# Kernel optimization log

Hardware: AMD Instinct MI355X
Metric: run time of the kernel (lower is better)

Reference implementation:

```python
import jax, jax.numpy as jnp
import numpy as np

B, S, DIM, HID = 2, 256, 128, 128
EPS = 1e-5

def _ln(t, w, b):
    mu = jnp.mean(t, axis=-1, keepdims=True)
    var = jnp.mean(jnp.square(t - mu), axis=-1, keepdims=True)
    return (t - mu) * jax.lax.rsqrt(var + EPS) * w + b

def setup_inputs() -> dict:
    key = jax.random.key(0)
    ks = jax.random.split(key, 8)
    sc = 1.0 / np.sqrt(DIM)
    return {
        "x": jax.random.normal(ks[0], (B, S, S, DIM), dtype=jnp.float32),
        "mask": jax.random.uniform(ks[1], (B, S, S), dtype=jnp.float32),
        "norm_w": jnp.ones((DIM,), jnp.float32),
        "norm_b": jnp.zeros((DIM,), jnp.float32),
        "w_left": jax.random.uniform(ks[2], (HID, DIM), jnp.float32, -sc, sc),
        "w_right": jax.random.uniform(ks[3], (HID, DIM), jnp.float32, -sc, sc),
        "w_lg": jax.random.uniform(ks[4], (HID, DIM), jnp.float32, -sc, sc),
        "w_rg": jax.random.uniform(ks[5], (HID, DIM), jnp.float32, -sc, sc),
        "w_og": jax.random.uniform(ks[6], (HID, DIM), jnp.float32, -sc, sc),
        "out_norm_w": jnp.ones((HID,), jnp.float32),
        "out_norm_b": jnp.zeros((HID,), jnp.float32),
        "w_out": jax.random.uniform(ks[7], (DIM, HID), jnp.float32, -1.0 / np.sqrt(HID), 1.0 / np.sqrt(HID)),
    }

def reference(x, mask, norm_w, norm_b, w_left, w_right, w_lg, w_rg, w_og,
              out_norm_w, out_norm_b, w_out):
    xn = _ln(x, norm_w, norm_b)                      # [B,S,S,D]
    m = mask[..., None]                              # [B,S,S,1]
    left = (xn @ w_left.T) * m * jax.nn.sigmoid(xn @ w_lg.T)    # [B,S,S,H]
    right = (xn @ w_right.T) * m * jax.nn.sigmoid(xn @ w_rg.T)  # [B,S,S,H]
    out_gate = jax.nn.sigmoid(xn @ w_og.T)
    # torch: permute to [B,H,S,S], bf16 bmm, permute back -> out[b,i,j,h] = sum_k L[b,i,k,h]*R[b,j,k,h]
    out = jnp.einsum("bikh,bjkh->bijh",
                     left.astype(jnp.bfloat16), right.astype(jnp.bfloat16),
                     preferred_element_type=jnp.float32)
    out = out.astype(jnp.bfloat16).astype(jnp.float32)
    out = _ln(out, out_norm_w, out_norm_b) * out_gate
    return out @ w_out.T                             # [B,S,S,D]
```

## Files before the change

kernel.cpp:

```cpp
#include <hip/hip_runtime.h>


#define SS 256
#define DD 128
#define HH 128

typedef __attribute__((ext_vector_type(8))) short bf16x8;
typedef __attribute__((ext_vector_type(4))) float f32x4;

__device__ __forceinline__ unsigned short f2b(float f) {
  unsigned u = __builtin_bit_cast(unsigned, f);
  u = (u + 0x7FFFu + ((u >> 16) & 1u)) >> 16;
  return (unsigned short)u;
}
__device__ __forceinline__ float b2f(unsigned short h) {
  return __builtin_bit_cast(float, ((unsigned)h) << 16);
}
__device__ __forceinline__ float sigmoidf_(float x) {
  return 1.0f / (1.0f + expf(-x));
}

__global__ __launch_bounds__(1024) void k_cvt(
    const float* __restrict__ s0, const float* __restrict__ s1,
    const float* __restrict__ s2, const float* __restrict__ s3,
    const float* __restrict__ s4, const float* __restrict__ s5,
    unsigned short* __restrict__ dst)
{
  int m = blockIdx.x >> 4;
  int e = ((blockIdx.x & 15) << 10) | threadIdx.x;
  const float* s = (m == 0) ? s0 : (m == 1) ? s1 : (m == 2) ? s2
                 : (m == 3) ? s3 : (m == 4) ? s4 : s5;
  dst[m * 16384 + e] = f2b(s[e]);
}

__global__ __launch_bounds__(256, 4) void k_stage1(
    const float* __restrict__ x, const float* __restrict__ mask,
    const float* __restrict__ nw, const float* __restrict__ nb,
    const unsigned short* __restrict__ wb,
    unsigned short* __restrict__ Lt, unsigned short* __restrict__ Rt,
    unsigned short* __restrict__ og)
{
  __shared__ unsigned short xnS[64][136];
  __shared__ unsigned short oS[128][72];
  __shared__ float maskS[64];

  const int tid  = threadIdx.x;
  const int wave = tid >> 6, lane = tid & 63;
  const int quad = lane >> 4, l16 = lane & 15;
  const int r0 = blockIdx.x * 64;
  const int bq = r0 >> 16, iq = (r0 >> 8) & 255, j0 = r0 & 255;

  if (tid < 64) maskS[tid] = mask[r0 + tid];

  const float w0 = nw[lane], w1 = nw[lane + 64];
  const float b0 = nb[lane], b1 = nb[lane + 64];
  float v0a[16], v1a[16];
  #pragma unroll
  for (int rr = 0; rr < 16; ++rr) {
    const float* xr = x + (size_t)(r0 + wave * 16 + rr) * DD;
    v0a[rr] = xr[lane];
    v1a[rr] = xr[lane + 64];
  }
  #pragma unroll
  for (int rr = 0; rr < 16; ++rr) {
    int r = wave * 16 + rr;
    float v0 = v0a[rr], v1 = v1a[rr];
    float s = v0 + v1;
    #pragma unroll
    for (int o = 32; o; o >>= 1) s += __shfl_xor(s, o);
    float mu = s * (1.0f / 128.0f);
    float d0 = v0 - mu, d1 = v1 - mu;
    float q = d0 * d0 + d1 * d1;
    #pragma unroll
    for (int o = 32; o; o >>= 1) q += __shfl_xor(q, o);
    float rs = rsqrtf(q * (1.0f / 128.0f) + 1e-5f);
    xnS[r][lane]      = f2b(d0 * rs * w0 + b0);
    xnS[r][lane + 64] = f2b(d1 * rs * w1 + b1);
  }
  __syncthreads();

  const int h0 = wave * 32;
  const int jl = quad * 4;

  auto coopStore = [&](unsigned short* dstBase) {
    int h = tid >> 1, half = tid & 1;
    const bf16x8* s = (const bf16x8*)&oS[h][half * 32];
    bf16x8* d = (bf16x8*)(dstBase +
        ((((size_t)bq * 128 + h) * 256 + iq) * 256 + j0 + half * 32));
    d[0] = s[0]; d[1] = s[1]; d[2] = s[2]; d[3] = s[3];
  };

  auto gatedSection = [&](const unsigned short* __restrict__ Wv,
                          const unsigned short* __restrict__ Wg) {
    const unsigned short* pv = Wv + (h0 + l16) * 128 + quad * 8;
    const unsigned short* pg = Wg + (h0 + l16) * 128 + quad * 8;
    f32x4 aV[4][2], aG[4][2];
    #pragma unroll
    for (int rt = 0; rt < 4; ++rt)
      #pragma unroll
      for (int n = 0; n < 2; ++n) {
        aV[rt][n] = f32x4{0.f, 0.f, 0.f, 0.f};
        aG[rt][n] = f32x4{0.f, 0.f, 0.f, 0.f};
      }
    bf16x8 bv[2], bg[2], bvn[2], bgn[2];
    #pragma unroll
    for (int n = 0; n < 2; ++n) {
      bv[n] = *(const bf16x8*)(pv + n * 2048);
      bg[n] = *(const bf16x8*)(pg + n * 2048);
    }
    #pragma unroll
    for (int kk = 0; kk < 4; ++kk) {
      if (kk < 3) {
        #pragma unroll
        for (int n = 0; n < 2; ++n) {
          bvn[n] = *(const bf16x8*)(pv + n * 2048 + (kk + 1) * 32);
          bgn[n] = *(const bf16x8*)(pg + n * 2048 + (kk + 1) * 32);
        }
      }
      #pragma unroll
      for (int rt = 0; rt < 4; ++rt) {
        bf16x8 a = *(const bf16x8*)&xnS[rt * 16 + l16][kk * 32 + quad * 8];
        #pragma unroll
        for (int n = 0; n < 2; ++n) {
          aG[rt][n] = __builtin_amdgcn_mfma_f32_16x16x32_bf16(a, bg[n], aG[rt][n], 0, 0, 0);
          aV[rt][n] = __builtin_amdgcn_mfma_f32_16x16x32_bf16(a, bv[n], aV[rt][n], 0, 0, 0);
        }
      }
      #pragma unroll
      for (int n = 0; n < 2; ++n) { bv[n] = bvn[n]; bg[n] = bgn[n]; }
    }
    #pragma unroll
    for (int rt = 0; rt < 4; ++rt)
      #pragma unroll
      for (int n = 0; n < 2; ++n)
        #pragma unroll
        for (int rg = 0; rg < 4; ++rg) {
          float g = sigmoidf_(aG[rt][n][rg]);
          oS[h0 + n * 16 + l16][rt * 16 + jl + rg] =
              f2b(aV[rt][n][rg] * maskS[rt * 16 + jl + rg] * g);
        }
  };

  gatedSection(wb + 0 * 16384, wb + 2 * 16384);
  __syncthreads();
  coopStore(Lt);
  __syncthreads();

  gatedSection(wb + 1 * 16384, wb + 3 * 16384);
  __syncthreads();
  coopStore(Rt);
  __syncthreads();

  {
    const unsigned short* po = wb + 4 * 16384 + (h0 + l16) * 128 + quad * 8;
    f32x4 aO[4][2];
    #pragma unroll
    for (int rt = 0; rt < 4; ++rt)
      #pragma unroll
      for (int n = 0; n < 2; ++n) aO[rt][n] = f32x4{0.f, 0.f, 0.f, 0.f};
    bf16x8 bo[2], bon[2];
    #pragma unroll
    for (int n = 0; n < 2; ++n) bo[n] = *(const bf16x8*)(po + n * 2048);
    #pragma unroll
    for (int kk = 0; kk < 4; ++kk) {
      if (kk < 3) {
        #pragma unroll
        for (int n = 0; n < 2; ++n)
          bon[n] = *(const bf16x8*)(po + n * 2048 + (kk + 1) * 32);
      }
      #pragma unroll
      for (int rt = 0; rt < 4; ++rt) {
        bf16x8 a = *(const bf16x8*)&xnS[rt * 16 + l16][kk * 32 + quad * 8];
        #pragma unroll
        for (int n = 0; n < 2; ++n)
          aO[rt][n] = __builtin_amdgcn_mfma_f32_16x16x32_bf16(a, bo[n], aO[rt][n], 0, 0, 0);
      }
      #pragma unroll
      for (int n = 0; n < 2; ++n) bo[n] = bon[n];
    }
    unsigned short* ogS = &oS[0][0];
    #pragma unroll
    for (int rt = 0; rt < 4; ++rt)
      #pragma unroll
      for (int n = 0; n < 2; ++n)
        #pragma unroll
        for (int rg = 0; rg < 4; ++rg)
          ogS[(rt * 16 + jl + rg) * 136 + h0 + n * 16 + l16] =
              f2b(sigmoidf_(aO[rt][n][rg]));
  }
  __syncthreads();
  {
    int j = tid >> 2, qq = tid & 3;
    const bf16x8* s = (const bf16x8*)&oS[0][0] + 0;
    const unsigned short* ogS = &oS[0][0];
    const bf16x8* sp = (const bf16x8*)&ogS[j * 136 + qq * 32];
    bf16x8* d = (bf16x8*)(og + (size_t)(r0 + j) * HH + qq * 32);
    d[0] = sp[0]; d[1] = sp[1]; d[2] = sp[2]; d[3] = sp[3];
    (void)s;
  }
}

__global__ __launch_bounds__(256, 4) void k_stage2(
    const unsigned short* __restrict__ Lt, const unsigned short* __restrict__ Rt,
    unsigned short* __restrict__ Tt)
{
  __shared__ unsigned short As[128][72];
  __shared__ unsigned short Bs[128][72];

  const int tid  = threadIdx.x;
  const int wave = tid >> 6, lane = tid & 63;
  const int quad = lane >> 4, l16 = lane & 15;
  const int bh = blockIdx.y;
  const int it = blockIdx.x >> 1, jt = blockIdx.x & 1;

  const unsigned short* A  = Lt + (size_t)bh * 65536 + it * 128 * 256;
  const unsigned short* Bp = Rt + (size_t)bh * 65536 + jt * 128 * 256;

  f32x4 acc[2][8];
  #pragma unroll
  for (int mt = 0; mt < 2; ++mt)
    #pragma unroll
    for (int nt = 0; nt < 8; ++nt) acc[mt][nt] = f32x4{0.f, 0.f, 0.f, 0.f};

  const int srow = tid >> 3, sc8 = tid & 7;

  #pragma unroll
  for (int ks = 0; ks < 4; ++ks) {
    __syncthreads();
    #pragma unroll
    for (int i = 0; i < 4; ++i) {
      *(bf16x8*)&As[i * 32 + srow][sc8 * 8] =
          *(const bf16x8*)(A + (i * 32 + srow) * 256 + ks * 64 + sc8 * 8);
      *(bf16x8*)&Bs[i * 32 + srow][sc8 * 8] =
          *(const bf16x8*)(Bp + (i * 32 + srow) * 256 + ks * 64 + sc8 * 8);
    }
    __syncthreads();
    #pragma unroll
    for (int k2 = 0; k2 < 2; ++k2) {
      int ko = k2 * 32 + quad * 8;
      bf16x8 a0 = *(const bf16x8*)&As[wave * 32 + l16][ko];
      bf16x8 a1 = *(const bf16x8*)&As[wave * 32 + 16 + l16][ko];
      #pragma unroll
      for (int nt = 0; nt < 8; ++nt) {
        bf16x8 b = *(const bf16x8*)&Bs[nt * 16 + l16][ko];
        acc[0][nt] = __builtin_amdgcn_mfma_f32_16x16x32_bf16(a0, b, acc[0][nt], 0, 0, 0);
        acc[1][nt] = __builtin_amdgcn_mfma_f32_16x16x32_bf16(a1, b, acc[1][nt], 0, 0, 0);
      }
    }
  }

  unsigned short* C = Tt + (size_t)bh * 65536 + it * 128 * 256 + jt * 128;
  #pragma unroll
  for (int mt = 0; mt < 2; ++mt)
    #pragma unroll
    for (int nt = 0; nt < 8; ++nt)
      #pragma unroll
      for (int rg = 0; rg < 4; ++rg)
        C[(wave * 32 + mt * 16 + quad * 4 + rg) * 256 + nt * 16 + l16] = f2b(acc[mt][nt][rg]);
}

__global__ __launch_bounds__(256, 4) void k_stage3(
    const unsigned short* __restrict__ Tt, const unsigned short* __restrict__ og,
    const float* __restrict__ onw, const float* __restrict__ onb,
    const unsigned short* __restrict__ wbO, float* __restrict__ out)
{
  __shared__ unsigned short tS[128][72];
  __shared__ unsigned short vS[64][136];
  __shared__ float onwS[128], onbS[128];
  __shared__ float muS[64], rsS[64];

  const int tid  = threadIdx.x;
  const int wave = tid >> 6, lane = tid & 63;
  const int quad = lane >> 4, l16 = lane & 15;
  const int r0 = blockIdx.x * 64;
  const int bq = r0 >> 16, iq = (r0 >> 8) & 255, j0 = r0 & 255;

  if (tid < 128) { onwS[tid] = onw[tid]; onbS[tid] = onb[tid]; }

  {
    int h = tid >> 1, half = tid & 1;
    const bf16x8* s = (const bf16x8*)(Tt +
        ((((size_t)bq * 128 + h) * 256 + iq) * 256 + j0 + half * 32));
    bf16x8* d = (bf16x8*)&tS[h][half * 32];
    d[0] = s[0]; d[1] = s[1]; d[2] = s[2]; d[3] = s[3];
  }
  __syncthreads();

  {
    int j = lane;
    #pragma unroll
    for (int c = 0; c < 4; ++c) {
      bf16x8 t;
      #pragma unroll
      for (int e = 0; e < 8; ++e) t[e] = (short)tS[wave * 32 + c * 8 + e][j];
      *(bf16x8*)&vS[j][wave * 32 + c * 8] = t;
    }
  }
  __syncthreads();

  if (tid < 128) {
    int j = tid >> 1, h0 = (tid & 1) * 64;
    float s = 0.f, q = 0.f;
    #pragma unroll
    for (int h = 0; h < 64; ++h) {
      float v = b2f(vS[j][h0 + h]);
      s += v; q += v * v;
    }
    s += __shfl_xor(s, 1);
    q += __shfl_xor(q, 1);
    float mu = s * (1.0f / 128.0f);
    float var = q * (1.0f / 128.0f) - mu * mu;
    float rs = rsqrtf(var + 1e-5f);
    if ((tid & 1) == 0) { muS[j] = mu; rsS[j] = rs; }
  }
  __syncthreads();

  {
    int j = tid >> 2, hq = tid & 3;
    float mu = muS[j], rs = rsS[j];
    const unsigned short* ogp = og + (size_t)(r0 + j) * HH + hq * 32;
    unsigned short* vp = &vS[j][hq * 32];
    #pragma unroll
    for (int c = 0; c < 4; ++c) {
      bf16x8 tv = *(bf16x8*)&vp[c * 8];
      bf16x8 gv = *(const bf16x8*)(ogp + c * 8);
      bf16x8 r;
      #pragma unroll
      for (int e = 0; e < 8; ++e) {
        int hh = hq * 32 + c * 8 + e;
        float v = (b2f((unsigned short)tv[e]) - mu) * rs * onwS[hh] + onbS[hh];
        r[e] = (short)f2b(v * b2f((unsigned short)gv[e]));
      }
      *(bf16x8*)&vp[c * 8] = r;
    }
  }
  __syncthreads();

  f32x4 acc[8];
  #pragma unroll
  for (int nt = 0; nt < 8; ++nt) acc[nt] = f32x4{0.f, 0.f, 0.f, 0.f};
  #pragma unroll
  for (int kk = 0; kk < 4; ++kk) {
    bf16x8 a = *(const bf16x8*)&vS[wave * 16 + l16][kk * 32 + quad * 8];
    #pragma unroll
    for (int nt = 0; nt < 8; ++nt) {
      bf16x8 b = *(const bf16x8*)(wbO + (nt * 16 + l16) * 128 + kk * 32 + quad * 8);
      acc[nt] = __builtin_amdgcn_mfma_f32_16x16x32_bf16(a, b, acc[nt], 0, 0, 0);
    }
  }
  #pragma unroll
  for (int nt = 0; nt < 8; ++nt)
    #pragma unroll
    for (int rg = 0; rg < 4; ++rg)
      out[(size_t)(r0 + wave * 16 + quad * 4 + rg) * DD + nt * 16 + l16] = acc[nt][rg];
}

extern "C" void kernel_launch(void* const* d_in, const int* in_sizes, int n_in,
                              void* d_out, int out_size, void* d_ws, size_t ws_size,
                              hipStream_t stream)
{
  const float* x    = (const float*)d_in[0];
  const float* mask = (const float*)d_in[1];
  const float* nw   = (const float*)d_in[2];
  const float* nb   = (const float*)d_in[3];
  const float* wL   = (const float*)d_in[4];
  const float* wR   = (const float*)d_in[5];
  const float* wLG  = (const float*)d_in[6];
  const float* wRG  = (const float*)d_in[7];
  const float* wOG  = (const float*)d_in[8];
  const float* onw  = (const float*)d_in[9];
  const float* onb  = (const float*)d_in[10];
  const float* wO   = (const float*)d_in[11];

  char* ws = (char*)d_ws;
  unsigned short* wb = (unsigned short*)ws;
  unsigned short* og = (unsigned short*)(ws + (1 << 18));
  unsigned short* Lt = (unsigned short*)(ws + (1 << 18) + 1 * (size_t)(1 << 25));
  unsigned short* Rt = (unsigned short*)(ws + (1 << 18) + 2 * (size_t)(1 << 25));
  unsigned short* Tt = (unsigned short*)(ws + (1 << 18) + 3 * (size_t)(1 << 25));

  k_cvt<<<96, 1024, 0, stream>>>(wL, wR, wLG, wRG, wOG, wO, wb);
  k_stage1<<<2048, 256, 0, stream>>>(x, mask, nw, nb, wb, Lt, Rt, og);
  k_stage2<<<dim3(4, 256), 256, 0, stream>>>(Lt, Rt, Tt);
  k_stage3<<<2048, 256, 0, stream>>>(Tt, og, onw, onb, wb + 5 * 16384, (float*)d_out);
}
```

Baseline: 275.2 us.

## Prefetch stage2 tiles into registers, remap blocks per XCD, make stage3 wave-local

Stage2 now loads the next K-slice from global memory into registers while MFMAs run on the current shared-memory tile. It also remaps block indices so blocks sharing the same L/R panels land on the same XCD, aiming for better L2 reuse. Stage3 is restructured so each wave owns its 16 rows end to end: layer-norm stats are computed per wave and passed by shuffle, the gate load is prefetched early, and block-wide barriers become waitcnt fences. This cuts synchronisation and latency, at the cost of higher register pressure and a reliance on wave-local data ownership for correctness.

```diff
diff --git a/kernel.cpp b/kernel.cpp
--- a/kernel.cpp
+++ b/kernel.cpp
@@ -191,12 +191,10 @@
   __syncthreads();
   {
     int j = tid >> 2, qq = tid & 3;
-    const bf16x8* s = (const bf16x8*)&oS[0][0] + 0;
     const unsigned short* ogS = &oS[0][0];
     const bf16x8* sp = (const bf16x8*)&ogS[j * 136 + qq * 32];
     bf16x8* d = (bf16x8*)(og + (size_t)(r0 + j) * HH + qq * 32);
     d[0] = sp[0]; d[1] = sp[1]; d[2] = sp[2]; d[3] = sp[3];
-    (void)s;
   }
 }
 
@@ -210,8 +208,14 @@
   const int tid  = threadIdx.x;
   const int wave = tid >> 6, lane = tid & 63;
   const int quad = lane >> 4, l16 = lane & 15;
-  const int bh = blockIdx.y;
-  const int it = blockIdx.x >> 1, jt = blockIdx.x & 1;
+
+  const int w   = blockIdx.y * 4 + blockIdx.x;
+  const int grp = w >> 4;
+  const int xcd = w & 7;
+  const int jt  = (w >> 3) & 1;
+  const int pid = grp * 8 + xcd;
+  const int bh  = pid >> 1;
+  const int it  = pid & 1;
 
   const unsigned short* A  = Lt + (size_t)bh * 65536 + it * 128 * 256;
   const unsigned short* Bp = Rt + (size_t)bh * 65536 + jt * 128 * 256;
@@ -224,17 +228,28 @@
 
   const int srow = tid >> 3, sc8 = tid & 7;
 
+  bf16x8 ra[4], rb[4];
+  #pragma unroll
+  for (int i = 0; i < 4; ++i) {
+    ra[i] = *(const bf16x8*)(A  + (i * 32 + srow) * 256 + sc8 * 8);
+    rb[i] = *(const bf16x8*)(Bp + (i * 32 + srow) * 256 + sc8 * 8);
+  }
+
   #pragma unroll
   for (int ks = 0; ks < 4; ++ks) {
+    #pragma unroll
+    for (int i = 0; i < 4; ++i) {
+      *(bf16x8*)&As[i * 32 + srow][sc8 * 8] = ra[i];
+      *(bf16x8*)&Bs[i * 32 + srow][sc8 * 8] = rb[i];
+    }
     __syncthreads();
-    #pragma unroll
-    for (int i = 0; i < 4; ++i) {
-      *(bf16x8*)&As[i * 32 + srow][sc8 * 8] =
-          *(const bf16x8*)(A + (i * 32 + srow) * 256 + ks * 64 + sc8 * 8);
-      *(bf16x8*)&Bs[i * 32 + srow][sc8 * 8] =
-          *(const bf16x8*)(Bp + (i * 32 + srow) * 256 + ks * 64 + sc8 * 8);
-    }
-    __syncthreads();
+    if (ks < 3) {
+      #pragma unroll
+      for (int i = 0; i < 4; ++i) {
+        ra[i] = *(const bf16x8*)(A  + (i * 32 + srow) * 256 + (ks + 1) * 64 + sc8 * 8);
+        rb[i] = *(const bf16x8*)(Bp + (i * 32 + srow) * 256 + (ks + 1) * 64 + sc8 * 8);
+      }
+    }
     #pragma unroll
     for (int k2 = 0; k2 < 2; ++k2) {
       int ko = k2 * 32 + quad * 8;
@@ -247,6 +262,7 @@
         acc[1][nt] = __builtin_amdgcn_mfma_f32_16x16x32_bf16(a1, b, acc[1][nt], 0, 0, 0);
       }
     }
+    __syncthreads();
   }
 
   unsigned short* C = Tt + (size_t)bh * 65536 + it * 128 * 256 + jt * 128;
@@ -267,13 +283,21 @@
   __shared__ unsigned short tS[128][72];
   __shared__ unsigned short vS[64][136];
   __shared__ float onwS[128], onbS[128];
-  __shared__ float muS[64], rsS[64];
 
   const int tid  = threadIdx.x;
   const int wave = tid >> 6, lane = tid & 63;
   const int quad = lane >> 4, l16 = lane & 15;
   const int r0 = blockIdx.x * 64;
   const int bq = r0 >> 16, iq = (r0 >> 8) & 255, j0 = r0 & 255;
+  const int jw = wave * 16;
+
+  const int jE = jw + (lane >> 2), hq = lane & 3;
+  bf16x8 gpre[4];
+  {
+    const unsigned short* ogp = og + (size_t)(r0 + jE) * HH + hq * 32;
+    #pragma unroll
+    for (int c = 0; c < 4; ++c) gpre[c] = *(const bf16x8*)(ogp + c * 8);
+  }
 
   if (tid < 128) { onwS[tid] = onw[tid]; onbS[tid] = onb[tid]; }
 
@@ -287,43 +311,46 @@
   __syncthreads();
 
   {
-    int j = lane;
+    int j = jw + (lane & 15);
+    int hb = (lane >> 4) * 32;
     #pragma unroll
     for (int c = 0; c < 4; ++c) {
       bf16x8 t;
       #pragma unroll
-      for (int e = 0; e < 8; ++e) t[e] = (short)tS[wave * 32 + c * 8 + e][j];
-      *(bf16x8*)&vS[j][wave * 32 + c * 8] = t;
-    }
-  }
-  __syncthreads();
-
-  if (tid < 128) {
-    int j = tid >> 1, h0 = (tid & 1) * 64;
+      for (int e = 0; e < 8; ++e) t[e] = (short)tS[hb + c * 8 + e][j];
+      *(bf16x8*)&vS[j][hb + c * 8] = t;
+    }
+  }
+  asm volatile("s_waitcnt lgkmcnt(0)" ::: "memory");
+
+  float mu, rs;
+  {
+    int j = jw + ((lane & 31) >> 1), h0 = (lane & 1) * 64;
     float s = 0.f, q = 0.f;
     #pragma unroll
-    for (int h = 0; h < 64; ++h) {
-      float v = b2f(vS[j][h0 + h]);
-      s += v; q += v * v;
+    for (int c = 0; c < 8; ++c) {
+      bf16x8 v8 = *(const bf16x8*)&vS[j][h0 + c * 8];
+      #pragma unroll
+      for (int e = 0; e < 8; ++e) {
+        float v = b2f((unsigned short)v8[e]);
+        s += v; q += v * v;
+      }
     }
     s += __shfl_xor(s, 1);
     q += __shfl_xor(q, 1);
-    float mu = s * (1.0f / 128.0f);
+    mu = s * (1.0f / 128.0f);
     float var = q * (1.0f / 128.0f) - mu * mu;
-    float rs = rsqrtf(var + 1e-5f);
-    if ((tid & 1) == 0) { muS[j] = mu; rsS[j] = rs; }
-  }
-  __syncthreads();
-
-  {
-    int j = tid >> 2, hq = tid & 3;
-    float mu = muS[j], rs = rsS[j];
-    const unsigned short* ogp = og + (size_t)(r0 + j) * HH + hq * 32;
-    unsigned short* vp = &vS[j][hq * 32];
+    rs = rsqrtf(var + 1e-5f);
+  }
+  mu = __shfl(mu, (jE - jw) << 1);
+  rs = __shfl(rs, (jE - jw) << 1);
+
+  {
+    unsigned short* vp = &vS[jE][hq * 32];
     #pragma unroll
     for (int c = 0; c < 4; ++c) {
       bf16x8 tv = *(bf16x8*)&vp[c * 8];
-      bf16x8 gv = *(const bf16x8*)(ogp + c * 8);
+      bf16x8 gv = gpre[c];
       bf16x8 r;
       #pragma unroll
       for (int e = 0; e < 8; ++e) {
@@ -334,14 +361,14 @@
       *(bf16x8*)&vp[c * 8] = r;
     }
   }
-  __syncthreads();
+  asm volatile("s_waitcnt lgkmcnt(0)" ::: "memory");
 
   f32x4 acc[8];
   #pragma unroll
   for (int nt = 0; nt < 8; ++nt) acc[nt] = f32x4{0.f, 0.f, 0.f, 0.f};
   #pragma unroll
   for (int kk = 0; kk < 4; ++kk) {
-    bf16x8 a = *(const bf16x8*)&vS[wave * 16 + l16][kk * 32 + quad * 8];
+    bf16x8 a = *(const bf16x8*)&vS[jw + l16][kk * 32 + quad * 8];
     #pragma unroll
     for (int nt = 0; nt < 8; ++nt) {
       bf16x8 b = *(const bf16x8*)(wbO + (nt * 16 + l16) * 128 + kk * 32 + quad * 8);
@@ -352,7 +379,7 @@
   for (int nt = 0; nt < 8; ++nt)
     #pragma unroll
     for (int rg = 0; rg < 4; ++rg)
-      out[(size_t)(r0 + wave * 16 + quad * 4 + rg) * DD + nt * 16 + l16] = acc[nt][rg];
+      out[(size_t)(r0 + jw + quad * 4 + rg) * DD + nt * 16 + l16] = acc[nt][rg];
 }
 
 extern "C" void kernel_launch(void* const* d_in, const int* in_sizes, int n_in,
```

Result: no change. 276.1 us (+0.3%).
